# Performance work log

Hardware: AMD Instinct MI355X
Metric: run time of the kernel (lower is better)

## Reference

```python
import jax, jax.numpy as jnp
import numpy as np

B = 4096          # batch
L = 4096          # lattice_size (64x64)
N = L // 2        # n_masked
H = 2048          # hidden_size


def setup_inputs() -> dict:
    key = jax.random.key(0)
    ks = jax.random.split(key, 4)
    scale = 0.02  # small init so exp(s) stays tame (s is already bounded by 2*tanh)
    x = jax.random.normal(ks[0], (B, L), dtype=jnp.float32)
    W1 = jax.random.normal(ks[1], (N, H), dtype=jnp.float32) * scale
    b1 = jnp.zeros((H,), jnp.float32)
    W2 = jax.random.normal(ks[2], (H, H), dtype=jnp.float32) * scale
    b2 = jnp.zeros((H,), jnp.float32)
    W3 = jax.random.normal(ks[3], (H, 2 * N), dtype=jnp.float32) * scale
    b3 = jnp.zeros((2 * N,), jnp.float32)
    # checkerboard mask: even sites frozen (masked), odd sites transformed
    idx_masked = jnp.arange(0, L, 2, dtype=jnp.int32)
    idx_unmasked = jnp.arange(1, L, 2, dtype=jnp.int32)
    return {"x": x, "W1": W1, "b1": b1, "W2": W2, "b2": b2,
            "W3": W3, "b3": b3,
            "idx_masked": idx_masked, "idx_unmasked": idx_unmasked}


def reference(x, W1, b1, W2, b2, W3, b3, idx_masked, idx_unmasked):
    # gather frozen half: (B, N)
    x_m = x[:, idx_masked]
    # 3-layer MLP with LeakyReLU(0.2)
    h = jax.nn.leaky_relu(x_m @ W1 + b1, negative_slope=0.2)
    h = jax.nn.leaky_relu(h @ W2 + b2, negative_slope=0.2)
    out = h @ W3 + b3                      # (B, 2N)
    s, t = out[:, :N], out[:, N:]
    s = 2.0 * jnp.tanh(s)
    # affine transform of the unmasked half, scatter back
    x_u = x[:, idx_unmasked]
    y_u = x_u * jnp.exp(s) + t
    y = x.at[:, idx_unmasked].set(y_u)
    log_det = s.sum(axis=1)                # (B,)
    return y, log_det
```

## Files before the change

### kernel.cpp

```cpp
#include <hip/hip_runtime.h>
#include <hip/hip_bf16.h>
#include <stdint.h>

#define MROWS 4096
#define LFULL 4096
#define NHALF 2048
#define HDIM  2048

typedef __bf16 bf16x8 __attribute__((ext_vector_type(8)));
typedef float  f32x4  __attribute__((ext_vector_type(4)));
typedef unsigned short u16x8 __attribute__((ext_vector_type(8)));

template<int V> struct ICt { static constexpr int value = V; };

__device__ __forceinline__ unsigned short f2bf(float f) {
    __hip_bfloat16 h = __float2bfloat16(f);
    return __builtin_bit_cast(unsigned short, h);
}
__device__ __forceinline__ float bf2f(unsigned short u) {
    return __builtin_bit_cast(float, (uint32_t)u << 16);
}
__device__ __forceinline__ float fast_tanh(float x) {
    float ax = fabsf(x);
    float e  = __expf(-2.0f * ax);
    float t  = (1.0f - e) / (1.0f + e);
    return copysignf(t, x);
}

__device__ __forceinline__ void gload_lds16(const void* g, void* l) {
    __builtin_amdgcn_global_load_lds(
        (const __attribute__((address_space(1))) uint32_t*)g,
        (__attribute__((address_space(3))) uint32_t*)l,
        16, 0, 0);
}

__global__ __launch_bounds__(256)
void cast_x_kernel(const float* __restrict__ x, __hip_bfloat16* __restrict__ xm)
{
    size_t t = (size_t)blockIdx.x * 256 + threadIdx.x;
    size_t r = t >> 8;
    int    c = (int)(t & 255);
    const float4* xp = (const float4*)(x + r * LFULL + (size_t)c * 16);
    float4 a = xp[0], b = xp[1], d = xp[2], e = xp[3];
    u16x8 v;
    v[0] = f2bf(a.x); v[1] = f2bf(a.z);
    v[2] = f2bf(b.x); v[3] = f2bf(b.z);
    v[4] = f2bf(d.x); v[5] = f2bf(d.z);
    v[6] = f2bf(e.x); v[7] = f2bf(e.z);
    *(u16x8*)(xm + r * NHALF + (size_t)c * 8) = v;
}

__global__ __launch_bounds__(256)
void transpose_cast_kernel(const float* __restrict__ W, __hip_bfloat16* __restrict__ WT,
                           int K, int N)
{
    __shared__ unsigned short lds[64][66];
    const int t  = threadIdx.x;
    const int k0 = blockIdx.y * 64;
    const int n0 = blockIdx.x * 64;

    #pragma unroll
    for (int it = 0; it < 4; ++it) {
        int kl = it * 16 + (t >> 4);
        int nl = (t & 15) * 4;
        float4 v = *(const float4*)(W + (size_t)(k0 + kl) * N + n0 + nl);
        lds[kl][nl + 0] = f2bf(v.x);
        lds[kl][nl + 1] = f2bf(v.y);
        lds[kl][nl + 2] = f2bf(v.z);
        lds[kl][nl + 3] = f2bf(v.w);
    }
    __syncthreads();

    int nl = t >> 2;
    int kc = (t & 3) * 16;
    unsigned short tmp[16];
    #pragma unroll
    for (int j = 0; j < 16; ++j) tmp[j] = lds[kc + j][nl];
    u16x8* dst = (u16x8*)(WT + (size_t)(n0 + nl) * K + k0 + kc);
    dst[0] = *(u16x8*)&tmp[0];
    dst[1] = *(u16x8*)&tmp[8];
}

template<int BM, int BN, int KD, int NOUT, bool RELU>
__global__ __launch_bounds__(512, 2)
void gemm8p(const __hip_bfloat16* __restrict__ A,
            const __hip_bfloat16* __restrict__ BT,
            const float* __restrict__ bias,
            __hip_bfloat16* __restrict__ C)
{
    constexpr int MF = BM / 32, NF = BN / 64, MH = MF / 2, NH = NF / 2;
    constexpr int LA = BM / 128, LB = BN / 128;
    constexpr int NT = KD / 64;
    constexpr int ABYTES = BM * 128, BBYTES = BN * 128;
    constexpr int BBASE = 2 * ABYTES;
    __shared__ __align__(1024) char lds[2 * ABYTES + 2 * BBYTES];

    const int tid  = threadIdx.x;
    const int wave = tid >> 6, lane = tid & 63;
    const int wm = wave >> 2, wn = wave & 3;
    const int l15 = lane & 15, lhi = lane >> 4;

    const int nwg = gridDim.x;
    const int bid = blockIdx.x;
    const int wg  = (bid & 7) * (nwg >> 3) + (bid >> 3);
    constexpr int NBN = NOUT / BN;
    const int bm = wg / NBN, bn = wg % NBN;

    const __hip_bfloat16* gA = A  + (size_t)(bm * BM) * KD;
    const __hip_bfloat16* gB = BT + (size_t)(bn * BN) * KD;

    const int srow = tid >> 3;
    const int scol = ((tid & 7) ^ (srow & 7)) * 8;
    char* sd = lds + srow * 128 + (tid & 7) * 16;

    const __hip_bfloat16* pA = gA + (size_t)srow * KD + scol;
    const __hip_bfloat16* pB = gB + (size_t)srow * KD + scol;

    #pragma unroll
    for (int s = 0; s < LB; ++s) gload_lds16(pB + (size_t)(s * 64) * KD,             sd + BBASE + s * 8192);
    #pragma unroll
    for (int s = 0; s < LB; ++s) gload_lds16(pB + (size_t)(BN/2 + s * 64) * KD,      sd + BBASE + (BN/2) * 128 + s * 8192);
    #pragma unroll
    for (int s = 0; s < LA; ++s) gload_lds16(pA + (size_t)(s * 64) * KD,             sd + s * 8192);
    #pragma unroll
    for (int s = 0; s < LA; ++s) gload_lds16(pA + (size_t)(BM/2 + s * 64) * KD,      sd + (BM/2) * 128 + s * 8192);
    #pragma unroll
    for (int s = 0; s < LB; ++s) gload_lds16(pB + 64 + (size_t)(s * 64) * KD,        sd + BBASE + BBYTES + s * 8192);
    #pragma unroll
    for (int s = 0; s < LB; ++s) gload_lds16(pB + 64 + (size_t)(BN/2 + s * 64) * KD, sd + BBASE + BBYTES + (BN/2) * 128 + s * 8192);
    pA += 64; pB += 128;
    asm volatile("s_waitcnt vmcnt(4)" ::: "memory");
    __builtin_amdgcn_s_barrier();

    const int arow0 = wm * (BM / 2) + l15;
    const int brow0 = wn * (BN / 4) + l15;
    const int swz   = (l15 & 7) << 4;
    const int colX[2] = { (lhi * 16) ^ swz, (64 + lhi * 16) ^ swz };
    const char* rA = lds + arow0 * 128;
    const char* rB = lds + brow0 * 128;

    bf16x8 af[MH][2], bf0[NH][2], bf1[NH][2];
    f32x4 acc[MF][NF] = {};

    #pragma unroll
    for (int m = 0; m < MH; ++m)
        #pragma unroll
        for (int kk = 0; kk < 2; ++kk)
            af[m][kk] = *(const bf16x8*)(rA + colX[kk] + m * 2048);
    #pragma unroll
    for (int n = 0; n < NH; ++n)
        #pragma unroll
        for (int kk = 0; kk < 2; ++kk)
            bf0[n][kk] = *(const bf16x8*)(rB + colX[kk] + (BBASE + n * 2048));

    auto body = [&](int t, auto bufc) {
        constexpr int BUF   = decltype(bufc)::value;
        constexpr int ABUF  = BUF * ABYTES;
        constexpr int ABUFo = (BUF ^ 1) * ABYTES;
        constexpr int BBUF  = BBASE + BUF * BBYTES;
        constexpr int BBUFo = BBASE + (BUF ^ 1) * BBYTES;

        if (t + 1 < NT) {
            #pragma unroll
            for (int s = 0; s < LA; ++s)
                gload_lds16(pA + (size_t)(s * 64) * KD, sd + ABUFo + s * 8192);
        }
        __builtin_amdgcn_s_setprio(1);
        #pragma unroll
        for (int kk = 0; kk < 2; ++kk)
            #pragma unroll
            for (int m = 0; m < MH; ++m)
                #pragma unroll
                for (int n = 0; n < NH; ++n)
                    acc[m][n] = __builtin_amdgcn_mfma_f32_16x16x32_bf16(af[m][kk], bf0[n][kk], acc[m][n], 0, 0, 0);
        __builtin_amdgcn_s_setprio(0);
        #pragma unroll
        for (int n = 0; n < NH; ++n)
            #pragma unroll
            for (int kk = 0; kk < 2; ++kk)
                bf1[n][kk] = *(const bf16x8*)(rB + colX[kk] + (BBUF + (NH + n) * 2048));
        __builtin_amdgcn_s_barrier();

        if (t + 1 < NT) {
            #pragma unroll
            for (int s = 0; s < LA; ++s)
                gload_lds16(pA + (size_t)(BM/2 + s * 64) * KD, sd + ABUFo + (BM/2) * 128 + s * 8192);
        }
        __builtin_amdgcn_s_setprio(1);
        #pragma unroll
        for (int kk = 0; kk < 2; ++kk)
            #pragma unroll
            for (int m = 0; m < MH; ++m)
                #pragma unroll
                for (int n = 0; n < NH; ++n)
                    acc[m][NH + n] = __builtin_amdgcn_mfma_f32_16x16x32_bf16(af[m][kk], bf1[n][kk], acc[m][NH + n], 0, 0, 0);
        __builtin_amdgcn_s_setprio(0);
        #pragma unroll
        for (int m = 0; m < MH; ++m)
            #pragma unroll
            for (int kk = 0; kk < 2; ++kk)
                af[m][kk] = *(const bf16x8*)(rA + colX[kk] + (ABUF + (MH + m) * 2048));
        __builtin_amdgcn_s_barrier();

        if (t + 2 < NT) {
            #pragma unroll
            for (int s = 0; s < LB; ++s)
                gload_lds16(pB + (size_t)(s * 64) * KD, sd + BBUF + s * 8192);
        }
        __builtin_amdgcn_s_setprio(1);
        #pragma unroll
        for (int kk = 0; kk < 2; ++kk)
            #pragma unroll
            for (int m = 0; m < MH; ++m)
                #pragma unroll
                for (int n = 0; n < NH; ++n)
                    acc[MH + m][n] = __builtin_amdgcn_mfma_f32_16x16x32_bf16(af[m][kk], bf0[n][kk], acc[MH + m][n], 0, 0, 0);
        __builtin_amdgcn_s_setprio(0);
        __builtin_amdgcn_s_barrier();

        if (t + 2 < NT) {
            #pragma unroll
            for (int s = 0; s < LB; ++s)
                gload_lds16(pB + (size_t)(BN/2 + s * 64) * KD, sd + BBUF + (BN/2) * 128 + s * 8192);
            asm volatile("s_waitcnt vmcnt(4)" ::: "memory");
        } else {
            asm volatile("s_waitcnt vmcnt(0)" ::: "memory");
        }
        __builtin_amdgcn_s_barrier();
        if (t + 1 < NT) {
            #pragma unroll
            for (int n = 0; n < NH; ++n)
                #pragma unroll
                for (int kk = 0; kk < 2; ++kk)
                    bf0[n][kk] = *(const bf16x8*)(rB + colX[kk] + (BBUFo + n * 2048));
        }
        __builtin_amdgcn_s_setprio(1);
        #pragma unroll
        for (int kk = 0; kk < 2; ++kk)
            #pragma unroll
            for (int m = 0; m < MH; ++m)
                #pragma unroll
                for (int n = 0; n < NH; ++n)
                    acc[MH + m][NH + n] = __builtin_amdgcn_mfma_f32_16x16x32_bf16(af[m][kk], bf1[n][kk], acc[MH + m][NH + n], 0, 0, 0);
        __builtin_amdgcn_s_setprio(0);
        if (t + 1 < NT) {
            #pragma unroll
            for (int m = 0; m < MH; ++m)
                #pragma unroll
                for (int kk = 0; kk < 2; ++kk)
                    af[m][kk] = *(const bf16x8*)(rA + colX[kk] + (ABUFo + m * 2048));
        }
        pA += 64; pB += 64;
    };

    for (int tt = 0; tt < NT; tt += 2) {
        body(tt,     ICt<0>{});
        body(tt + 1, ICt<1>{});
    }

    const int crow0 = bm * BM + wm * (BM / 2) + lhi * 4;
    const int ccol0 = bn * BN + wn * (BN / 4) + l15;
    #pragma unroll
    for (int m = 0; m < MF; ++m) {
        #pragma unroll
        for (int n = 0; n < NF; ++n) {
            int col = ccol0 + n * 16;
            float bv = bias[col];
            #pragma unroll
            for (int r = 0; r < 4; ++r) {
                int row = crow0 + m * 16 + r;
                float v = acc[m][n][r] + bv;
                if (RELU) v = (v > 0.0f) ? v : 0.2f * v;
                C[(size_t)row * NOUT + col] = __float2bfloat16(v);
            }
        }
    }
}

__global__ __launch_bounds__(256)
void epilogue_kernel(const float* __restrict__ x,
                     const __hip_bfloat16* __restrict__ outb,
                     float* __restrict__ y, float* __restrict__ ld)
{
    const int i = blockIdx.x;
    const int t = threadIdx.x;
    const __hip_bfloat16* orow = outb + (size_t)i * LFULL;
    const float* xrow = x + (size_t)i * LFULL;
    float* yrow = y + (size_t)i * LFULL;

    const int j0 = t * 8;
    u16x8 sv = *(const u16x8*)(orow + j0);
    u16x8 tv = *(const u16x8*)(orow + NHALF + j0);

    float part = 0.0f;
    #pragma unroll
    for (int u = 0; u < 8; u += 2) {
        float4 xv = *(const float4*)(xrow + 2 * (j0 + u));
        float s0 = bf2f(sv[u]),     s1 = bf2f(sv[u + 1]);
        float t0 = bf2f(tv[u]),     t1 = bf2f(tv[u + 1]);
        float a0 = 2.0f * fast_tanh(s0);
        float a1 = 2.0f * fast_tanh(s1);
        part += a0 + a1;
        float4 yv;
        yv.x = xv.x;  yv.y = xv.y * __expf(a0) + t0;
        yv.z = xv.z;  yv.w = xv.w * __expf(a1) + t1;
        *(float4*)(yrow + 2 * (j0 + u)) = yv;
    }

    #pragma unroll
    for (int off = 32; off; off >>= 1) part += __shfl_down(part, off, 64);
    __shared__ float red[4];
    if ((t & 63) == 0) red[t >> 6] = part;
    __syncthreads();
    if (t == 0) ld[i] = red[0] + red[1] + red[2] + red[3];
}

extern "C" void kernel_launch(void* const* d_in, const int* in_sizes, int n_in,
                              void* d_out, int out_size, void* d_ws, size_t ws_size,
                              hipStream_t stream)
{
    const float* x  = (const float*)d_in[0];
    const float* W1 = (const float*)d_in[1];
    const float* b1 = (const float*)d_in[2];
    const float* W2 = (const float*)d_in[3];
    const float* b2 = (const float*)d_in[4];
    const float* W3 = (const float*)d_in[5];
    const float* b3 = (const float*)d_in[6];

    char* ws = (char*)d_ws;
    const size_t MB = 1u << 20;
    __hip_bfloat16* W3T  = (__hip_bfloat16*)(ws);
    __hip_bfloat16* h2   = (__hip_bfloat16*)(ws + 16 * MB);
    __hip_bfloat16* xmb  = (__hip_bfloat16*)(ws + 32 * MB);
    __hip_bfloat16* W1T  = (__hip_bfloat16*)(ws + 48 * MB);
    __hip_bfloat16* W2T  = (__hip_bfloat16*)(ws + 56 * MB);
    __hip_bfloat16* h1   = (__hip_bfloat16*)(ws + 64 * MB);
    __hip_bfloat16* outb = (__hip_bfloat16*)(ws + 32 * MB);

    float* y  = (float*)d_out;
    float* ld = y + (size_t)MROWS * LFULL;

    cast_x_kernel<<<4096, 256, 0, stream>>>(x, xmb);
    transpose_cast_kernel<<<dim3(32, 32), 256, 0, stream>>>(W1, W1T, HDIM, HDIM);
    transpose_cast_kernel<<<dim3(32, 32), 256, 0, stream>>>(W2, W2T, HDIM, HDIM);
    transpose_cast_kernel<<<dim3(64, 32), 256, 0, stream>>>(W3, W3T, HDIM, LFULL);

    gemm8p<128, 256, 2048, 2048, true ><<<dim3(256), dim3(512), 0, stream>>>(xmb, W1T, b1, h1);
    gemm8p<128, 256, 2048, 2048, true ><<<dim3(256), dim3(512), 0, stream>>>(h1,  W2T, b2, h2);
    gemm8p<256, 256, 2048, 4096, false><<<dim3(256), dim3(512), 0, stream>>>(h2,  W3T, b3, outb);

    epilogue_kernel<<<4096, 256, 0, stream>>>(x, outb, y, ld);
}
```

Before: 198.0 us.

## Fuse coupling epilogue into third GEMM via permuted W3 columns

W3 columns are permuted during the transpose so that each GEMM tile holds matching s and t columns. This lets the affine coupling, the tanh/exp and the log-det reduction run directly in the third GEMM's epilogue, with the log-det accumulated through atomics. The separate epilogue kernel and the bf16 round-trip of the 4096x4096 output are removed, and log_det is zeroed in the cast kernel. In exchange the GEMM epilogue does strided float2 reads and writes of x and y plus atomic adds, and s and t stay in fp32 instead of being rounded to bf16.

```diff
diff --git a/kernel.cpp b/kernel.cpp
--- a/kernel.cpp
+++ b/kernel.cpp
@@ -35,8 +35,10 @@
 }
 
 __global__ __launch_bounds__(256)
-void cast_x_kernel(const float* __restrict__ x, __hip_bfloat16* __restrict__ xm)
+void cast_x_kernel(const float* __restrict__ x, __hip_bfloat16* __restrict__ xm,
+                   float* __restrict__ ld)
 {
+    if (threadIdx.x == 0) ld[blockIdx.x] = 0.0f;
     size_t t = (size_t)blockIdx.x * 256 + threadIdx.x;
     size_t r = t >> 8;
     int    c = (int)(t & 255);
@@ -50,6 +52,7 @@
     *(u16x8*)(xm + r * NHALF + (size_t)c * 8) = v;
 }
 
+template<bool PERM>
 __global__ __launch_bounds__(256)
 void transpose_cast_kernel(const float* __restrict__ W, __hip_bfloat16* __restrict__ WT,
                            int K, int N)
@@ -76,17 +79,31 @@
     unsigned short tmp[16];
     #pragma unroll
     for (int j = 0; j < 16; ++j) tmp[j] = lds[kc + j][nl];
-    u16x8* dst = (u16x8*)(WT + (size_t)(n0 + nl) * K + k0 + kc);
+    int jc = n0 + nl;
+    int dstrow;
+    if (PERM) {
+        int half = jc >> 11;
+        int j    = jc & 2047;
+        int g = j >> 7, w = j & 127;
+        int q = w >> 5, rest = w & 31, f = rest >> 4, c = rest & 15;
+        dstrow = g * 256 + q * 64 + (f + 2 * half) * 16 + c;
+    } else {
+        dstrow = jc;
+    }
+    u16x8* dst = (u16x8*)(WT + (size_t)dstrow * K + k0 + kc);
     dst[0] = *(u16x8*)&tmp[0];
     dst[1] = *(u16x8*)&tmp[8];
 }
 
-template<int BM, int BN, int KD, int NOUT, bool RELU>
+template<int BM, int BN, int KD, int NOUT, bool RELU, bool FUSED>
 __global__ __launch_bounds__(512, 2)
 void gemm8p(const __hip_bfloat16* __restrict__ A,
             const __hip_bfloat16* __restrict__ BT,
             const float* __restrict__ bias,
-            __hip_bfloat16* __restrict__ C)
+            __hip_bfloat16* __restrict__ C,
+            const float* __restrict__ xg,
+            float* __restrict__ yg,
+            float* __restrict__ ldg)
 {
     constexpr int MF = BM / 32, NF = BN / 64, MH = MF / 2, NH = NF / 2;
     constexpr int LA = BM / 128, LB = BN / 128;
@@ -258,61 +275,54 @@
         body(tt + 1, ICt<1>{});
     }
 
-    const int crow0 = bm * BM + wm * (BM / 2) + lhi * 4;
-    const int ccol0 = bn * BN + wn * (BN / 4) + l15;
-    #pragma unroll
-    for (int m = 0; m < MF; ++m) {
-        #pragma unroll
-        for (int n = 0; n < NF; ++n) {
-            int col = ccol0 + n * 16;
-            float bv = bias[col];
+    if constexpr (FUSED) {
+        const int crow0 = bm * BM + wm * (BM / 2) + lhi * 4;
+        const int jbase = bn * (BN / 2) + wn * 32 + l15;
+        #pragma unroll
+        for (int m = 0; m < MF; ++m) {
             #pragma unroll
             for (int r = 0; r < 4; ++r) {
-                int row = crow0 + m * 16 + r;
-                float v = acc[m][n][r] + bv;
-                if (RELU) v = (v > 0.0f) ? v : 0.2f * v;
-                C[(size_t)row * NOUT + col] = __float2bfloat16(v);
+                const int row = crow0 + m * 16 + r;
+                float ldp = 0.0f;
+                #pragma unroll
+                for (int n = 0; n < 2; ++n) {
+                    const int j = jbase + n * 16;
+                    float sval = acc[m][n][r]     + bias[j];
+                    float tval = acc[m][n + 2][r] + bias[NHALF + j];
+                    float a = 2.0f * fast_tanh(sval);
+                    ldp += a;
+                    float2 xv = *(const float2*)(xg + (size_t)row * LFULL + 2 * j);
+                    float2 yv;
+                    yv.x = xv.x;
+                    yv.y = xv.y * __expf(a) + tval;
+                    *(float2*)(yg + (size_t)row * LFULL + 2 * j) = yv;
+                }
+                ldp += __shfl_xor(ldp, 1, 64);
+                ldp += __shfl_xor(ldp, 2, 64);
+                ldp += __shfl_xor(ldp, 4, 64);
+                ldp += __shfl_xor(ldp, 8, 64);
+                if (l15 == 0) atomicAdd(&ldg[row], ldp);
             }
         }
+    } else {
+        const int crow0 = bm * BM + wm * (BM / 2) + lhi * 4;
+        const int ccol0 = bn * BN + wn * (BN / 4) + l15;
+        #pragma unroll
+        for (int m = 0; m < MF; ++m) {
+            #pragma unroll
+            for (int n = 0; n < NF; ++n) {
+                int col = ccol0 + n * 16;
+                float bv = bias[col];
+                #pragma unroll
+                for (int r = 0; r < 4; ++r) {
+                    int row = crow0 + m * 16 + r;
+                    float v = acc[m][n][r] + bv;
+                    if (RELU) v = (v > 0.0f) ? v : 0.2f * v;
+                    C[(size_t)row * NOUT + col] = __float2bfloat16(v);
+                }
+            }
+        }
     }
-}
-
-__global__ __launch_bounds__(256)
-void epilogue_kernel(const float* __restrict__ x,
-                     const __hip_bfloat16* __restrict__ outb,
-                     float* __restrict__ y, float* __restrict__ ld)
-{
-    const int i = blockIdx.x;
-    const int t = threadIdx.x;
-    const __hip_bfloat16* orow = outb + (size_t)i * LFULL;
-    const float* xrow = x + (size_t)i * LFULL;
-    float* yrow = y + (size_t)i * LFULL;
-
-    const int j0 = t * 8;
-    u16x8 sv = *(const u16x8*)(orow + j0);
-    u16x8 tv = *(const u16x8*)(orow + NHALF + j0);
-
-    float part = 0.0f;
-    #pragma unroll
-    for (int u = 0; u < 8; u += 2) {
-        float4 xv = *(const float4*)(xrow + 2 * (j0 + u));
-        float s0 = bf2f(sv[u]),     s1 = bf2f(sv[u + 1]);
-        float t0 = bf2f(tv[u]),     t1 = bf2f(tv[u + 1]);
-        float a0 = 2.0f * fast_tanh(s0);
-        float a1 = 2.0f * fast_tanh(s1);
-        part += a0 + a1;
-        float4 yv;
-        yv.x = xv.x;  yv.y = xv.y * __expf(a0) + t0;
-        yv.z = xv.z;  yv.w = xv.w * __expf(a1) + t1;
-        *(float4*)(yrow + 2 * (j0 + u)) = yv;
-    }
-
-    #pragma unroll
-    for (int off = 32; off; off >>= 1) part += __shfl_down(part, off, 64);
-    __shared__ float red[4];
-    if ((t & 63) == 0) red[t >> 6] = part;
-    __syncthreads();
-    if (t == 0) ld[i] = red[0] + red[1] + red[2] + red[3];
 }
 
 extern "C" void kernel_launch(void* const* d_in, const int* in_sizes, int n_in,
@@ -335,19 +345,16 @@
     __hip_bfloat16* W1T  = (__hip_bfloat16*)(ws + 48 * MB);
     __hip_bfloat16* W2T  = (__hip_bfloat16*)(ws + 56 * MB);
     __hip_bfloat16* h1   = (__hip_bfloat16*)(ws + 64 * MB);
-    __hip_bfloat16* outb = (__hip_bfloat16*)(ws + 32 * MB);
 
     float* y  = (float*)d_out;
     float* ld = y + (size_t)MROWS * LFULL;
 
-    cast_x_kernel<<<4096, 256, 0, stream>>>(x, xmb);
-    transpose_cast_kernel<<<dim3(32, 32), 256, 0, stream>>>(W1, W1T, HDIM, HDIM);
-    transpose_cast_kernel<<<dim3(32, 32), 256, 0, stream>>>(W2, W2T, HDIM, HDIM);
-    transpose_cast_kernel<<<dim3(64, 32), 256, 0, stream>>>(W3, W3T, HDIM, LFULL);
-
-    gemm8p<128, 256, 2048, 2048, true ><<<dim3(256), dim3(512), 0, stream>>>(xmb, W1T, b1, h1);
-    gemm8p<128, 256, 2048, 2048, true ><<<dim3(256), dim3(512), 0, stream>>>(h1,  W2T, b2, h2);
-    gemm8p<256, 256, 2048, 4096, false><<<dim3(256), dim3(512), 0, stream>>>(h2,  W3T, b3, outb);
-
-    epilogue_kernel<<<4096, 256, 0, stream>>>(x, outb, y, ld);
-}
+    cast_x_kernel<<<4096, 256, 0, stream>>>(x, xmb, ld);
+    transpose_cast_kernel<false><<<dim3(32, 32), 256, 0, stream>>>(W1, W1T, HDIM, HDIM);
+    transpose_cast_kernel<false><<<dim3(32, 32), 256, 0, stream>>>(W2, W2T, HDIM, HDIM);
+    transpose_cast_kernel<true ><<<dim3(64, 32), 256, 0, stream>>>(W3, W3T, HDIM, LFULL);
+
+    gemm8p<128, 256, 2048, 2048, true,  false><<<dim3(256), dim3(512), 0, stream>>>(xmb, W1T, b1, h1, nullptr, nullptr, nullptr);
+    gemm8p<128, 256, 2048, 2048, true,  false><<<dim3(256), dim3(512), 0, stream>>>(h1,  W2T, b2, h2, nullptr, nullptr, nullptr);
+    gemm8p<256, 256, 2048, 4096, false, true ><<<dim3(256), dim3(512), 0, stream>>>(h2,  W3T, b3, nullptr, x, y, ld);
+}
```

Measured after the change: 184.8 us. -6.6%, faster.
